# Kernel tuning notes

Hardware: AMD Instinct MI355X
Metric: run time of the kernel (lower is better)

The kernel has to match this reference:

```python
import jax, jax.numpy as jnp
import numpy as np

B, HGRID, D_MODEL = 4, 64, 96
D_INNER, D_STATE, DT_RANK, K = 192, 16, 6, 4
L = HGRID * HGRID


def setup_inputs() -> dict:
    key = jax.random.key(0)
    ks = jax.random.split(key, 12)
    C, N, R, D = D_INNER, D_STATE, DT_RANK, D_MODEL
    s = 0.02
    x = jax.random.normal(ks[0], (B, L, D), jnp.float32)
    in_proj_w = jax.random.normal(ks[1], (2 * C, D)) * s
    fft_w1 = jax.random.normal(ks[2], (C, C)) * s
    fft_b1 = jnp.zeros((C,))
    fft_w2 = jax.random.normal(ks[3], (C, C)) * s
    fft_b2 = jnp.zeros((C,))
    wave_w = jax.random.normal(ks[4], (C, C, 3, 3)) * s
    wave_b = jnp.zeros((C,))
    dw_w = jax.random.normal(ks[5], (C, 1, 3, 3)) * 0.1
    dw_b = jnp.zeros((C,))
    sym_w = jnp.asarray(0.3, jnp.float32)
    x_proj_w = jax.random.normal(ks[6], (K, R + 2 * N, C)) * s
    dt_std = R ** -0.5
    dt_w = jax.random.uniform(ks[7], (K, C, R), minval=-dt_std, maxval=dt_std)
    dt = jnp.exp(jax.random.uniform(ks[8], (K, C)) * (np.log(0.1) - np.log(0.001)) + np.log(0.001))
    dt = jnp.maximum(dt, 1e-4)
    dt_b = dt + jnp.log(-jnp.expm1(-dt))  # inverse softplus init as in dt_init
    A_logs = jnp.log(jnp.tile(jnp.arange(1, N + 1, dtype=jnp.float32), (K * C, 1)))  # [K*C, N]
    Ds = jnp.ones((K * C,))
    out_norm_g = jnp.ones((C,))
    out_norm_b = jnp.zeros((C,))
    out_proj_w = jax.random.normal(ks[9], (D, C)) * s
    rms_w = jnp.ones((D,))
    return dict(x=x, in_proj_w=in_proj_w, fft_w1=fft_w1, fft_b1=fft_b1, fft_w2=fft_w2,
                fft_b2=fft_b2, wave_w=wave_w, wave_b=wave_b, dw_w=dw_w, dw_b=dw_b,
                sym_w=sym_w, x_proj_w=x_proj_w, dt_w=dt_w, dt_b=dt_b, A_logs=A_logs,
                Ds=Ds, out_norm_g=out_norm_g, out_norm_b=out_norm_b,
                out_proj_w=out_proj_w, rms_w=rms_w)


def _conv2d(x, w, b, groups=1):
    y = jax.lax.conv_general_dilated(x, w, (1, 1), 'SAME', feature_group_count=groups,
                                     dimension_numbers=('NCHW', 'OIHW', 'NCHW'))
    return y + b[None, :, None, None]


def _haar_dwt(x):
    # orthonormal single-level Haar on 2x2 blocks
    a = x[..., 0::2, 0::2]; b = x[..., 0::2, 1::2]
    c = x[..., 1::2, 0::2]; d = x[..., 1::2, 1::2]
    return ((a + b + c + d) * 0.5, (a - b + c - d) * 0.5,
            (a + b - c - d) * 0.5, (a - b - c + d) * 0.5)


def _haar_idwt(ll, lh, hl, hh):
    a = (ll + lh + hl + hh) * 0.5; b = (ll - lh + hl - hh) * 0.5
    c = (ll + lh - hl - hh) * 0.5; d = (ll - lh - hl + hh) * 0.5
    Bb, Cc, H2, W2 = ll.shape
    top = jnp.stack([a, b], -1).reshape(Bb, Cc, H2, 2 * W2)
    bot = jnp.stack([c, d], -1).reshape(Bb, Cc, H2, 2 * W2)
    return jnp.stack([top, bot], -2).reshape(Bb, Cc, 2 * H2, 2 * W2)


def _freq_model(x, fft_w1, fft_b1, fft_w2, fft_b2, wave_w, wave_b):
    Bb, C, H, W = x.shape
    xf = jnp.fft.rfft2(x, norm='ortho')
    m = jax.nn.gelu(jnp.einsum('bchw,oc->bohw', jnp.abs(xf), fft_w1)
                    + fft_b1[None, :, None, None], approximate=False)
    mag = jnp.einsum('bchw,oc->bohw', m, fft_w2) + fft_b2[None, :, None, None]
    x_fourier = jnp.fft.irfft2(mag * jnp.exp(1j * jnp.angle(xf)), s=(H, W), norm='ortho')
    ll, lh, hl, hh = _haar_dwt(x)
    lh = _conv2d(lh, wave_w, wave_b)
    hl = _conv2d(hl, wave_w, wave_b)
    hh = _conv2d(hh, wave_w, wave_b)
    x_wavelet = _haar_idwt(ll, lh, hl, hh)
    return x + x_fourier + x_wavelet


def _selective_scan(xs, delta, A, Bs, Cs, Ds):
    # xs/delta: [B,K,C,L]; A: [K,C,N]; Bs/Cs: [B,K,N,L]; Ds: [K,C]
    Bb, Kk, C, Ll = xs.shape
    N = A.shape[-1]
    u_t = jnp.moveaxis(xs, -1, 0)     # [L,B,K,C]
    d_t = jnp.moveaxis(delta, -1, 0)
    B_t = jnp.moveaxis(Bs, -1, 0)     # [L,B,K,N]
    C_t = jnp.moveaxis(Cs, -1, 0)

    def step(h, inp):
        u, dd, bb, cc = inp
        h = jnp.exp(dd[..., None] * A) * h + (dd * u)[..., None] * bb[:, :, None, :]
        return h, jnp.einsum('bkcn,bkn->bkc', h, cc)

    h0 = jnp.zeros((Bb, Kk, C, N), xs.dtype)
    _, ys = jax.lax.scan(step, h0, (u_t, d_t, B_t, C_t))
    return jnp.moveaxis(ys, 0, -1) + xs * Ds[None, :, :, None]


def _forward(x, in_proj_w, fft_w1, fft_b1, fft_w2, fft_b2, wave_w, wave_b, dw_w, dw_b,
             sym_w, x_proj_w, dt_w, dt_b, A_logs, Ds, out_norm_g, out_norm_b,
             out_proj_w, rms_w):
    Bb, Ll, D = x.shape
    H = W = HGRID
    C, N, R = D_INNER, D_STATE, DT_RANK
    # RMSNorm (residual pre-norm)
    xn = x * jax.lax.rsqrt(jnp.mean(x * x, -1, keepdims=True) + 1e-5) * rms_w
    xz = xn.reshape(Bb, H, W, D) @ in_proj_w.T            # [B,H,W,2C]
    xi, z = jnp.split(xz, 2, axis=-1)
    xc = jnp.transpose(xi, (0, 3, 1, 2))                  # NCHW
    xc = xc + _freq_model(xc, fft_w1, fft_b1, fft_w2, fft_b2, wave_w, wave_b)
    a = jax.nn.silu(_conv2d(xc, dw_w, dw_b, groups=C))    # depthwise 3x3
    # 4-direction sequences
    x_flat = a.reshape(Bb, C, Ll)
    x_t = jnp.transpose(a, (0, 1, 3, 2)).reshape(Bb, C, Ll)
    xs = jnp.stack([x_flat, x_t, x_flat[..., ::-1], x_t[..., ::-1]], axis=1)  # [B,4,C,L]
    x_dbl = jnp.einsum('bkdl,kcd->bkcl', xs, x_proj_w)
    dts, Bs, Cs = jnp.split(x_dbl, [R, R + N], axis=2)
    dts = jnp.einsum('bkrl,kdr->bkdl', dts, dt_w)
    delta = jax.nn.softplus(dts + dt_b[None, :, :, None])
    A = -jnp.exp(A_logs).reshape(K, C, N)
    out_y = _selective_scan(xs, delta, A, Bs, Cs, Ds.reshape(K, C))  # [B,4,C,L]
    wh = jnp.transpose(out_y[:, 1].reshape(Bb, C, W, H), (0, 1, 3, 2)).reshape(Bb, C, Ll)
    iwh = jnp.transpose(out_y[:, 3, :, ::-1].reshape(Bb, C, W, H), (0, 1, 3, 2)).reshape(Bb, C, Ll)
    y = out_y[:, 0] + out_y[:, 2, :, ::-1] + wh + iwh     # [B,C,L]
    # lightweight symmetry enhancement
    y4 = y.reshape(Bb, C, H, W)
    wgt = jax.nn.sigmoid(sym_w)
    enh = y4 * (1 - wgt) + 0.5 * (y4 + y4[..., ::-1]) * wgt
    yf = y + 0.2 * enh.reshape(Bb, C, Ll)
    yf = jnp.transpose(yf, (0, 2, 1)).reshape(Bb, H, W, C)
    # LayerNorm
    mu = yf.mean(-1, keepdims=True)
    var = ((yf - mu) ** 2).mean(-1, keepdims=True)
    yn = (yf - mu) * jax.lax.rsqrt(var + 1e-5) * out_norm_g + out_norm_b
    out = (yn * jax.nn.silu(z)) @ out_proj_w.T
    return out.reshape(Bb, Ll, D) + x  # residual


def reference(x, in_proj_w, fft_w1, fft_b1, fft_w2, fft_b2, wave_w, wave_b, dw_w, dw_b,
              sym_w, x_proj_w, dt_w, dt_b, A_logs, Ds, out_norm_g, out_norm_b,
              out_proj_w, rms_w):
    return _forward(x, in_proj_w, fft_w1, fft_b1, fft_w2, fft_b2, wave_w, wave_b,
                    dw_w, dw_b, sym_w, x_proj_w, dt_w, dt_b, A_logs, Ds,
                    out_norm_g, out_norm_b, out_proj_w, rms_w)
```

## Files before the change

### kernel.cpp

```cpp
#include <hip/hip_runtime.h>
#include <hip/hip_bf16.h>

#define CI 192
#define LL_ 4096

typedef __bf16 v8bf __attribute__((ext_vector_type(8)));
typedef float  v4f  __attribute__((ext_vector_type(4)));
typedef float  v8f  __attribute__((ext_vector_type(8)));
typedef unsigned short v8us __attribute__((ext_vector_type(8)));

__device__ __forceinline__ unsigned short f2bf(float v){
  unsigned int u = __float_as_uint(v);
  return (unsigned short)((u + 0x7FFFu + ((u >> 16) & 1u)) >> 16);
}

__global__ __launch_bounds__(256) void k_zero(float* __restrict__ p, int n){
  int i = blockIdx.x*256 + threadIdx.x;
  if (i < n) p[i] = 0.f;
}

__global__ __launch_bounds__(256) void k_rms_inproj(const float* __restrict__ x,
    const float* __restrict__ rmsw, const float* __restrict__ ipw,
    float* __restrict__ xc, float* __restrict__ zT){
  int og = blockIdx.x & 7; int lt = (blockIdx.x >> 3) & 63; int b = blockIdx.x >> 9;
  int l0 = lt << 6;
  __shared__ float xt[64][97];
  __shared__ float wt[96*48];
  __shared__ float rr[64];
  __shared__ float rw[96];
  int tid = threadIdx.x;
  for (int idx = tid; idx < 6144; idx += 256){ int r = idx/96, d = idx - r*96;
    xt[r][d] = x[((size_t)b*4096 + l0 + r)*96 + d]; }
  if (tid < 96) rw[tid] = rmsw[tid];
  int o0 = og*48;
  for (int idx = tid; idx < 4608; idx += 256){ int o = idx%48, d = idx/48;
    wt[d*48 + o] = ipw[(size_t)(o0 + o)*96 + d]; }
  __syncthreads();
  if (tid < 64){
    float s = 0.f;
    for (int d = 0; d < 96; d++){ float v = xt[tid][d]; s += v*v; }
    rr[tid] = rsqrtf(s*(1.0f/96.0f) + 1e-5f);
  }
  __syncthreads();
  for (int idx = tid; idx < 6144; idx += 256){ int r = idx/96, d = idx - r*96;
    xt[r][d] *= rr[r]*rw[d]; }
  __syncthreads();
  int l = tid & 63, grp = tid >> 6;
  float acc[12];
  #pragma unroll
  for (int j = 0; j < 12; j++) acc[j] = 0.f;
  for (int d = 0; d < 96; d++){
    float xv = xt[l][d];
    const float* wr = &wt[d*48 + grp*12];
    #pragma unroll
    for (int j = 0; j < 12; j += 4){
      float4 w4 = *(const float4*)&wr[j];
      acc[j]   += xv*w4.x; acc[j+1] += xv*w4.y;
      acc[j+2] += xv*w4.z; acc[j+3] += xv*w4.w;
    }
  }
  #pragma unroll
  for (int j = 0; j < 12; j++){
    int o = o0 + grp*12 + j;
    if (o < 192) xc[((size_t)b*192 + o)*4096 + l0 + l] = acc[j];
    else         zT[((size_t)b*192 + (o-192))*4096 + l0 + l] = acc[j];
  }
}

__global__ __launch_bounds__(256) void k_dft_fwd(const float* __restrict__ xc,
    float* __restrict__ fre, float* __restrict__ fim, float* __restrict__ fab,
    float* __restrict__ ll, float* __restrict__ lh, float* __restrict__ hl, float* __restrict__ hh){
  int plane = blockIdx.x;
  __shared__ float sxT[64*65];
  __shared__ float t1r[64*34], t1i[64*34];
  __shared__ float tabr[16], tabi[16];
  __shared__ float ct64[64], st64[64];
  int tid = threadIdx.x;
  const float* X = xc + (size_t)plane*4096;
  for (int i = tid; i < 4096; i += 256){ int h = i >> 6, w = i & 63; sxT[w*65 + h] = X[i]; }
  if (tid < 16){ tabr[tid] = cospif((float)tid/8.0f); tabi[tid] = -sinpif((float)tid/8.0f); }
  if (tid < 64){ ct64[tid] = cospif((float)tid/32.0f); st64[tid] = sinpif((float)tid/32.0f); }
  __syncthreads();
  {
    size_t qbase = (size_t)plane*1024;
    for (int idx = tid; idx < 1024; idx += 256){
      int y2 = idx >> 5, x2 = idx & 31;
      float a_ = sxT[(2*x2)*65 + 2*y2],     b_ = sxT[(2*x2+1)*65 + 2*y2];
      float c_ = sxT[(2*x2)*65 + 2*y2+1],   d_ = sxT[(2*x2+1)*65 + 2*y2+1];
      ll[qbase + idx] = (a_+b_+c_+d_)*0.5f; lh[qbase + idx] = (a_-b_+c_-d_)*0.5f;
      hl[qbase + idx] = (a_+b_-c_-d_)*0.5f; hh[qbase + idx] = (a_-b_-c_+d_)*0.5f;
    }
  }
  {
    int hp = tid & 31, g = tid >> 5;
    float a0r[4], a0i[4], a1r[4], a1i[4];
    #pragma unroll
    for (int j = 0; j < 4; j++){ a0r[j]=0.f; a0i[j]=0.f; a1r[j]=0.f; a1i[j]=0.f; }
    float s32_0 = 0.f, s32_1 = 0.f;
    for (int w = 0; w < 64; w++){
      float xv0 = sxT[w*65 + hp];
      float xv1 = sxT[w*65 + hp + 32];
      int m0 = (w*g) & 15;
      float twr = tabr[m0], twi = tabi[m0];
      int ms = w & 15;
      float str = tabr[ms], sti = tabi[ms];
      #pragma unroll
      for (int j = 0; j < 4; j++){
        a0r[j] += xv0*twr; a0i[j] += xv0*twi;
        a1r[j] += xv1*twr; a1i[j] += xv1*twi;
        float nr = twr*str - twi*sti;
        float ni = twr*sti + twi*str;
        twr = nr; twi = ni;
      }
      if (g == 0){ float sg = (w & 1) ? -1.f : 1.f; s32_0 += xv0*sg; s32_1 += xv1*sg; }
    }
    #pragma unroll
    for (int j = 0; j < 4; j++){
      int k = 4*g + j;
      t1r[hp*34 + k] = a0r[j];        t1i[hp*34 + k] = a0i[j];
      t1r[(hp+32)*34 + k] = a1r[j];   t1i[(hp+32)*34 + k] = a1i[j];
    }
    if (g == 0){
      t1r[hp*34 + 32] = s32_0;      t1i[hp*34 + 32] = 0.f;
      t1r[(hp+32)*34 + 32] = s32_1; t1i[(hp+32)*34 + 32] = 0.f;
    }
  }
  __syncthreads();
  {
    int fp = tid & 31, g = tid >> 5;
    float stepr = cospif((float)fp/32.0f), stepi = -sinpif((float)fp/32.0f);
    float a0r[4], a0i[4], a1r[4], a1i[4];
    #pragma unroll
    for (int j = 0; j < 4; j++){ a0r[j]=0.f; a0i[j]=0.f; a1r[j]=0.f; a1i[j]=0.f; }
    float b0r=0.f, b0i=0.f, b1r=0.f, b1i=0.f;
    for (int hb = 0; hb < 4; hb++){
      int m = ((hb*16)*fp) & 63;
      float twr = ct64[m], twi = -st64[m];
      for (int hh2 = 0; hh2 < 16; hh2++){
        int h = hb*16 + hh2;
        float sg = (h & 1) ? -1.f : 1.f;
        #pragma unroll
        for (int j = 0; j < 4; j++){
          float Tr = t1r[h*34 + 4*g + j], Ti = t1i[h*34 + 4*g + j];
          float pr = Tr*twr - Ti*twi;
          float pi = Tr*twi + Ti*twr;
          a0r[j] += pr; a0i[j] += pi;
          a1r[j] += sg*pr; a1i[j] += sg*pi;
        }
        if (g == 0){
          float Tr = t1r[h*34 + 32], Ti = t1i[h*34 + 32];
          float pr = Tr*twr - Ti*twi, pi = Tr*twi + Ti*twr;
          b0r += pr; b0i += pi; b1r += sg*pr; b1i += sg*pi;
        }
        float nr = twr*stepr - twi*stepi, ni = twr*stepi + twi*stepr;
        twr = nr; twi = ni;
      }
    }
    size_t base = (size_t)plane*2112;
    #pragma unroll
    for (int j = 0; j < 4; j++){
      int k = 4*g + j;
      float r0 = a0r[j]*(1.f/64.f), i0 = a0i[j]*(1.f/64.f);
      float r1 = a1r[j]*(1.f/64.f), i1 = a1i[j]*(1.f/64.f);
      fre[base + fp*33 + k] = r0; fim[base + fp*33 + k] = i0;
      fab[base + fp*33 + k] = sqrtf(r0*r0 + i0*i0);
      fre[base + (fp+32)*33 + k] = r1; fim[base + (fp+32)*33 + k] = i1;
      fab[base + (fp+32)*33 + k] = sqrtf(r1*r1 + i1*i1);
    }
    if (g == 0){
      float r0 = b0r*(1.f/64.f), i0 = b0i*(1.f/64.f);
      float r1 = b1r*(1.f/64.f), i1 = b1i*(1.f/64.f);
      fre[base + fp*33 + 32] = r0; fim[base + fp*33 + 32] = i0;
      fab[base + fp*33 + 32] = sqrtf(r0*r0 + i0*i0);
      fre[base + (fp+32)*33 + 32] = r1; fim[base + (fp+32)*33 + 32] = i1;
      fab[base + (fp+32)*33 + 32] = sqrtf(r1*r1 + i1*i1);
    }
  }
}

__global__ __launch_bounds__(256) void k_cmix1(const float* __restrict__ fab,
    const float* __restrict__ w1, const float* __restrict__ b1, float* __restrict__ m){
  int bid = blockIdx.x;
  int pt = bid % 9; int og = (bid/9) % 24; int b = bid/216;
  int tid = threadIdx.x;
  int p = pt*256 + tid; bool act = p < 2112;
  __shared__ float wl[192*8];
  for (int idx = tid; idx < 1536; idx += 256){ int o = idx & 7, c = idx >> 3;
    wl[c*8 + o] = w1[(size_t)(og*8 + o)*192 + c]; }
  __syncthreads();
  float acc[8];
  #pragma unroll
  for (int o = 0; o < 8; o++) acc[o] = b1[og*8 + o];
  const float* xb = fab + (size_t)b*CI*2112 + p;
  for (int c = 0; c < 192; c++){
    float xv = act ? xb[(size_t)c*2112] : 0.f;
    float4 wa = *(const float4*)&wl[c*8];
    float4 wb4 = *(const float4*)&wl[c*8 + 4];
    acc[0] += xv*wa.x;  acc[1] += xv*wa.y;  acc[2] += xv*wa.z;  acc[3] += xv*wa.w;
    acc[4] += xv*wb4.x; acc[5] += xv*wb4.y; acc[6] += xv*wb4.z; acc[7] += xv*wb4.w;
  }
  if (act){
    #pragma unroll
    for (int o = 0; o < 8; o++){
      float a = acc[o];
      m[((size_t)b*192 + og*8 + o)*2112 + p] = 0.5f*a*(1.0f + erff(a*0.70710678118654752f));
    }
  }
}

__global__ __launch_bounds__(256) void k_cmix2(const float* __restrict__ m,
    const float* __restrict__ w2, const float* __restrict__ bi2,
    float* __restrict__ fre, float* __restrict__ fim, const float* __restrict__ fab){
  int bid = blockIdx.x;
  int pt = bid % 9; int og = (bid/9) % 24; int b = bid/216;
  int tid = threadIdx.x;
  int p = pt*256 + tid; bool act = p < 2112;
  __shared__ float wl[192*8];
  for (int idx = tid; idx < 1536; idx += 256){ int o = idx & 7, c = idx >> 3;
    wl[c*8 + o] = w2[(size_t)(og*8 + o)*192 + c]; }
  __syncthreads();
  float acc[8];
  #pragma unroll
  for (int o = 0; o < 8; o++) acc[o] = bi2[og*8 + o];
  const float* xb = m + (size_t)b*CI*2112 + p;
  for (int c = 0; c < 192; c++){
    float xv = act ? xb[(size_t)c*2112] : 0.f;
    float4 wa = *(const float4*)&wl[c*8];
    float4 wb4 = *(const float4*)&wl[c*8 + 4];
    acc[0] += xv*wa.x;  acc[1] += xv*wa.y;  acc[2] += xv*wa.z;  acc[3] += xv*wa.w;
    acc[4] += xv*wb4.x; acc[5] += xv*wb4.y; acc[6] += xv*wb4.z; acc[7] += xv*wb4.w;
  }
  if (act){
    #pragma unroll
    for (int o = 0; o < 8; o++){
      size_t id = ((size_t)b*192 + og*8 + o)*2112 + p;
      float ab = fab[id];
      float re, im;
      if (ab > 1e-30f){ float sc = acc[o]/ab; re = sc*fre[id]; im = sc*fim[id]; }
      else { re = acc[o]; im = 0.f; }
      fre[id] = re; fim[id] = im;
    }
  }
}

__global__ __launch_bounds__(256) void k_cvt_w(const float* __restrict__ ww,
    unsigned short* __restrict__ wqb2){
  int idx = blockIdx.x*256 + threadIdx.x;
  if (idx >= 331776) return;
  int ic = idx % 192; int rest = idx / 192;
  int oc = rest % 192; int q = rest / 192;
  wqb2[idx] = f2bf(ww[((size_t)oc*192 + ic)*9 + q]);
}

__global__ __launch_bounds__(256) void k_prep_lhT(const float* __restrict__ lhb,
    unsigned short* __restrict__ lhT){
  int id = blockIdx.x*256 + threadIdx.x;
  int pix = id & 1023;
  int icg = (id >> 10) % 24;
  int img = id / 24576;
  const float* s = lhb + (size_t)img*196608 + (size_t)(icg*8)*1024 + pix;
  v8us v;
  #pragma unroll
  for (int j = 0; j < 8; j++) v[j] = f2bf(s[(size_t)j*1024]);
  *(v8us*)&lhT[((size_t)img*1024 + pix)*192 + icg*8] = v;
}

__global__ __launch_bounds__(256) void k_wconv_mfma(const unsigned short* __restrict__ lhT,
    const unsigned short* __restrict__ wqb2, float* __restrict__ wnew){
  int bid = blockIdx.x;
  int nt = bid % 3; int mt = (bid/3) & 15; int img = bid/48;
  int o0 = nt*64;
  __shared__ __align__(16) unsigned short sm_us[26112];
  unsigned short* Aband = sm_us;
  float* T = (float*)sm_us;
  int tid = threadIdx.x;
  int lane = tid & 63, wv = tid >> 6;
  int quad = lane >> 4, n16 = lane & 15;
  const unsigned short* wrow = wqb2 + ((size_t)(o0 + 16*wv + n16))*192 + quad*8;
  v8us bcur[6], bnxt[6];
  #pragma unroll
  for (int icc = 0; icc < 6; icc++) bcur[icc] = *(const v8us*)&wrow[icc*32];
  for (int i = tid; i < 3264; i += 256) ((v8us*)sm_us)[i] = (v8us){0,0,0,0,0,0,0,0};
  __syncthreads();
  const unsigned short* base = lhT + (size_t)img*196608;
  for (int idx = tid; idx < 3072; idx += 256){
    int r = idx / 768; int t = idx - r*768;
    int pc = t / 24;   int icg = t - pc*24;
    int gr = 2*mt - 1 + r;
    if (gr >= 0 && gr < 32){
      v8us v = *(const v8us*)&base[((size_t)gr*32 + pc)*192 + icg*8];
      int pix = r*34 + 1 + pc;
      *(v8us*)&Aband[pix*192 + ((icg*8) ^ ((pix & 7) << 3))] = v;
    }
  }
  __syncthreads();
  v4f acc[4];
  #pragma unroll
  for (int t2 = 0; t2 < 4; t2++) acc[t2] = (v4f){0.f,0.f,0.f,0.f};
  #pragma unroll
  for (int q = 0; q < 9; q++){
    int ky = q/3, kx = q - ky*3;
    if (q < 8){
      #pragma unroll
      for (int icc = 0; icc < 6; icc++)
        bnxt[icc] = *(const v8us*)&wrow[(size_t)(q+1)*36864 + icc*32];
    }
    #pragma unroll
    for (int icc = 0; icc < 6; icc++){
      int c0 = icc*32;
      v8bf bv = __builtin_bit_cast(v8bf, bcur[icc]);
      #pragma unroll
      for (int t2 = 0; t2 < 4; t2++){
        int mm = t2*16 + n16;
        int pix = ((mm >> 5) + ky)*34 + (mm & 31) + kx;
        const unsigned short* Ap = &Aband[pix*192 + ((c0 + quad*8) ^ ((pix & 7) << 3))];
        v8bf av = __builtin_bit_cast(v8bf, *(const v8us*)Ap);
        acc[t2] = __builtin_amdgcn_mfma_f32_16x16x32_bf16(av, bv, acc[t2], 0, 0, 0);
      }
    }
    #pragma unroll
    for (int icc = 0; icc < 6; icc++) bcur[icc] = bnxt[icc];
  }
  __syncthreads();
  #pragma unroll
  for (int t2 = 0; t2 < 4; t2++)
    #pragma unroll
    for (int r = 0; r < 4; r++)
      T[(16*t2 + quad*4 + r)*65 + 16*wv + n16] = acc[t2][r];
  __syncthreads();
  float* outb = wnew + (size_t)img*196608;
  for (int idx = tid; idx < 4096; idx += 256){
    int mm = idx & 63, oc = idx >> 6;
    outb[(size_t)(o0 + oc)*1024 + mt*64 + mm] = T[mm*65 + oc];
  }
}

__global__ __launch_bounds__(256) void k_ifwd(const float* __restrict__ fre2,
    const float* __restrict__ fim2, const float* __restrict__ xc,
    const float* __restrict__ ll, const float* __restrict__ wnew, const float* __restrict__ wb,
    const float* __restrict__ dww, const float* __restrict__ dwb,
    float* __restrict__ ab, float* __restrict__ aT){
  int plane = blockIdx.x;
  int c = plane % 192;
  __shared__ float sm[12992];
  float* gr  = sm;
  float* gi  = sm + 2176;
  float* ur  = sm + 4352;
  float* ui  = sm + 6528;
  float* sx2 = sm + 8704;
  float* t64r = sm + 12864; float* t64i = sm + 12928;
  float* scratch = sm;
  int tid = threadIdx.x;
  for (int i = tid; i < 2112; i += 256){
    size_t o = (size_t)plane*2112 + i;
    int f = i/33, k = i - f*33;
    gr[f*34 + k] = fre2[o]; gi[f*34 + k] = fim2[o];
  }
  if (tid < 64){ t64r[tid] = cospif((float)tid/32.0f); t64i[tid] = sinpif((float)tid/32.0f); }
  __syncthreads();
  {
    int hp = tid & 31, g = tid >> 5;
    float stepr = cospif((float)hp/32.0f), stepi = sinpif((float)hp/32.0f);
    float a0r[4], a0i[4], a1r[4], a1i[4];
    #pragma unroll
    for (int j = 0; j < 4; j++){ a0r[j]=0.f; a0i[j]=0.f; a1r[j]=0.f; a1i[j]=0.f; }
    float b0r=0.f, b0i=0.f, b1r=0.f, b1i=0.f;
    for (int fb = 0; fb < 4; fb++){
      int m = ((fb*16)*hp) & 63;
      float twr = t64r[m], twi = t64i[m];
      for (int ff = 0; ff < 16; ff++){
        int f = fb*16 + ff;
        float sg = (f & 1) ? -1.f : 1.f;
        #pragma unroll
        for (int j = 0; j < 4; j++){
          float Gr = gr[f*34 + 4*g + j], Gi = gi[f*34 + 4*g + j];
          float pr = Gr*twr - Gi*twi;
          float pi = Gr*twi + Gi*twr;
          a0r[j] += pr; a0i[j] += pi;
          a1r[j] += sg*pr; a1i[j] += sg*pi;
        }
        if (g == 0){
          float Gr = gr[f*34 + 32], Gi = gi[f*34 + 32];
          float pr = Gr*twr - Gi*twi, pi = Gr*twi + Gi*twr;
          b0r += pr; b0i += pi; b1r += sg*pr; b1i += sg*pi;
        }
        float nr = twr*stepr - twi*stepi, ni = twr*stepi + twi*stepr;
        twr = nr; twi = ni;
      }
    }
    __syncthreads();
    #pragma unroll
    for (int j = 0; j < 4; j++){
      int k = 4*g + j;
      float ck = (k == 0) ? (1.f/64.f) : (2.f/64.f);
      ur[hp*34 + k] = a0r[j]*ck;       ui[hp*34 + k] = a0i[j]*ck;
      ur[(hp+32)*34 + k] = a1r[j]*ck;  ui[(hp+32)*34 + k] = a1i[j]*ck;
    }
    if (g == 0){
      ur[hp*34 + 32] = b0r*(1.f/64.f);      ui[hp*34 + 32] = b0i*(1.f/64.f);
      ur[(hp+32)*34 + 32] = b1r*(1.f/64.f); ui[(hp+32)*34 + 32] = b1i*(1.f/64.f);
    }
  }
  __syncthreads();
  {
    int h = tid & 63, wg = tid >> 6;
    v8f accL = (v8f)0.f, accH = (v8f)0.f, twr, twi, sr, si;
    #pragma unroll
    for (int j = 0; j < 8; j++){
      int wl = 8*wg + j;
      sr[j] = t64r[wl]; si[j] = t64i[wl];
      twr[j] = 1.f; twi[j] = 0.f;
    }
    float acc32 = 0.f;
    for (int k = 0; k <= 32; k++){
      float Ur = ur[h*34 + k], Ui = ui[h*34 + k];
      if (wg == 0) acc32 += (k & 1) ? -Ur : Ur;
      v8f p = Ur*twr, q = Ui*twi;
      accL += p - q;
      accH += p + q;
      v8f nr = twr*sr - twi*si;
      v8f ni = twr*si + twi*sr;
      twr = nr; twi = ni;
    }
    #pragma unroll
    for (int j = 0; j < 8; j++){
      int wl = 8*wg + j;
      sx2[h*65 + wl] = accL[j];
      if (wl == 0) sx2[h*65 + 32] = acc32;
      else         sx2[h*65 + 64 - wl] = accH[j];
    }
  }
  __syncthreads();
  float bia = wb[c];
  for (int p = tid; p < 4096; p += 256){
    int h = p >> 6, w = p & 63;
    size_t q = (size_t)plane*1024 + (size_t)(h >> 1)*32 + (w >> 1);
    float LLv = ll[q];
    float LH = wnew[q] + bia;
    float HL = wnew[786432 + q] + bia;
    float HH = wnew[1572864 + q] + bia;
    float v;
    bool hb = (h & 1), wbit = (w & 1);
    if (!hb && !wbit)      v = (LLv + LH + HL + HH)*0.5f;
    else if (!hb && wbit)  v = (LLv - LH + HL - HH)*0.5f;
    else if (hb && !wbit)  v = (LLv + LH - HL - HH)*0.5f;
    else                   v = (LLv - LH - HL + HH)*0.5f;
    sx2[h*65 + w] = 2.0f*xc[(size_t)plane*4096 + p] + sx2[h*65 + w] + v;
  }
  __syncthreads();
  float wk[9];
  #pragma unroll
  for (int q = 0; q < 9; q++) wk[q] = dww[c*9 + q];
  float dbv = dwb[c];
  for (int p = tid; p < 4096; p += 256){
    int h = p >> 6, w = p & 63;
    float acc = dbv;
    #pragma unroll
    for (int ky = 0; ky < 3; ky++){
      int yy = h + ky - 1; if (yy < 0 || yy > 63) continue;
      #pragma unroll
      for (int kx = 0; kx < 3; kx++){
        int xx = w + kx - 1; if (xx < 0 || xx > 63) continue;
        acc += sx2[yy*65 + xx]*wk[ky*3 + kx];
      }
    }
    scratch[h*65 + w] = acc / (1.f + __expf(-acc));
  }
  __syncthreads();
  float* abp = ab + (size_t)plane*4096;
  float* aTp = aT + (size_t)plane*4096;
  for (int p = tid; p < 4096; p += 256){
    abp[p] = scratch[(p >> 6)*65 + (p & 63)];
    aTp[p] = scratch[(p & 63)*65 + (p >> 6)];
  }
}

__global__ __launch_bounds__(256) void k_xproj(const float* __restrict__ ab,
    const float* __restrict__ aT, const float* __restrict__ xpw,
    float* __restrict__ Bsb, float* __restrict__ Csb, float* __restrict__ dlsb,
    float* __restrict__ xsb){
  int bid = blockIdx.x;
  int s = bid & 63; int k = (bid >> 6) & 3; int b = bid >> 8;
  int tid = threadIdx.x;
  __shared__ float als[192][65];
  __shared__ float dls[6][64];
  int l0 = s << 6;
  const float* src = (k & 1) ? aT : ab;
  bool rev = (k >= 2);
  for (int idx = tid; idx < 3072; idx += 256){
    int d = idx >> 4, i4 = idx & 15;
    const float* rowp = src + ((size_t)b*192 + d)*4096;
    if (!rev){
      float4 v = *(const float4*)&rowp[l0 + 4*i4];
      als[d][4*i4+0] = v.x; als[d][4*i4+1] = v.y;
      als[d][4*i4+2] = v.z; als[d][4*i4+3] = v.w;
    } else {
      float4 v = *(const float4*)&rowp[4092 - l0 - 4*i4];
      als[d][4*i4+0] = v.w; als[d][4*i4+1] = v.z;
      als[d][4*i4+2] = v.y; als[d][4*i4+3] = v.x;
    }
  }
  __syncthreads();
  {
    int i = tid & 63, wg = tid >> 6;
    const float* wr[10];
    #pragma unroll
    for (int r = 0; r < 10; r++){
      int cp = wg + 4*r; if (cp > 37) cp = 37;
      int off = __builtin_amdgcn_readfirstlane((k*38 + cp)*192);
      wr[r] = xpw + off;
    }
    float acc[10];
    #pragma unroll
    for (int r = 0; r < 10; r++) acc[r] = 0.f;
    for (int d = 0; d < 192; d++){
      float v = als[d][i];
      #pragma unroll
      for (int r = 0; r < 10; r++) acc[r] += v*wr[r][d];
    }
    #pragma unroll
    for (int r = 0; r < 10; r++){
      int cp = wg + 4*r;
      if (cp > 37) continue;
      if (cp < 6) dls[cp][i] = acc[r];
      else if (cp < 22) Bsb[((size_t)(b*4 + k)*16 + (cp - 6 ))*4096 + l0 + i] = acc[r];
      else              Csb[((size_t)(b*4 + k)*16 + (cp - 22))*4096 + l0 + i] = acc[r];
    }
  }
  size_t xbase = ((size_t)(b*4 + k)*4096 + l0)*192;
  for (int j = tid; j < 3072; j += 256){
    int i = j / 48, c4 = (j - (j/48)*48)*4;
    float4 v;
    v.x = als[c4+0][i]; v.y = als[c4+1][i];
    v.z = als[c4+2][i]; v.w = als[c4+3][i];
    *(float4*)&xsb[xbase + (size_t)i*192 + c4] = v;
  }
  __syncthreads();
  size_t dbase = (size_t)((b*4 + k)*64 + s)*384;
  for (int j = tid; j < 384; j += 256){
    int i = j/6, r = j - i*6;
    dlsb[dbase + j] = dls[r][i];
  }
}

__global__ __launch_bounds__(192) void k_scanA(const float* __restrict__ xsb,
    const float* __restrict__ dlsb, const float* __restrict__ Bsb,
    const float* __restrict__ dtw, const float* __restrict__ dtb,
    const float* __restrict__ alog, float* __restrict__ Pb, float* __restrict__ Qb){
  int bid = blockIdx.x; int s = bid & 63; int k = (bid >> 6) & 3; int b = bid >> 8;
  int c = threadIdx.x; int bk = b*4 + k;
  __shared__ float sdl[384];
  __shared__ float sB[16][64];
  size_t dbase = (size_t)(bk*64 + s)*384;
  for (int j = c; j < 384; j += 192) sdl[j] = dlsb[dbase + j];
  for (int j = c; j < 1024; j += 192){ int n = j >> 6, i = j & 63;
    sB[n][i] = Bsb[((size_t)bk*16 + n)*4096 + (s << 6) + i]; }
  __syncthreads();
  float A[16], P[16], Q[16];
  const float* arow = alog + ((size_t)k*192 + c)*16;
  bool fast = true;
  #pragma unroll
  for (int n = 0; n < 16; n++){
    A[n] = -__expf(arow[n]); P[n] = 1.f; Q[n] = 0.f;
    if (fabsf(A[n] + (float)(n+1)) > 1e-3f) fast = false;
  }
  float dw[6];
  #pragma unroll
  for (int r = 0; r < 6; r++) dw[r] = dtw[((size_t)k*192 + c)*6 + r];
  float db = dtb[k*192 + c];
  const float* xrow = xsb + ((size_t)bk*4096 + (s << 6))*192 + c;
  if (fast){
    for (int i = 0; i < 64; i++){
      float u = xrow[(size_t)i*192];
      float acc = db;
      #pragma unroll
      for (int r = 0; r < 6; r++) acc += sdl[i*6 + r]*dw[r];
      float ec = __expf(fminf(acc, 80.f));
      float dl = __logf(1.f + ec);
      float e1 = __builtin_amdgcn_rcpf(1.f + ec);
      float du = dl*u;
      float e = 1.f;
      #pragma unroll
      for (int n = 0; n < 16; n++){
        e *= e1;
        P[n] *= e;
        Q[n] = Q[n]*e + du*sB[n][i];
      }
    }
  } else {
    for (int i = 0; i < 64; i++){
      float u = xrow[(size_t)i*192];
      float acc = db;
      #pragma unroll
      for (int r = 0; r < 6; r++) acc += sdl[i*6 + r]*dw[r];
      float ec = __expf(fminf(acc, 80.f));
      float dl = __logf(1.f + ec);
      float du = dl*u;
      #pragma unroll
      for (int n = 0; n < 16; n++){
        float e = __expf(dl*A[n]);
        P[n] *= e;
        Q[n] = Q[n]*e + du*sB[n][i];
      }
    }
  }
  size_t pbase = ((size_t)(bk*64 + s)*16)*192 + c;
  #pragma unroll
  for (int n = 0; n < 16; n++){ Pb[pbase + (size_t)n*192] = P[n]; Qb[pbase + (size_t)n*192] = Q[n]; }
}

__global__ __launch_bounds__(256) void k_scanB(float* __restrict__ Pb,
    const float* __restrict__ Qb){
  int id = blockIdx.x*256 + threadIdx.x;
  int c = id % 192; int rest = id / 192; int n = rest % 16; int bk = rest / 16;
  float h = 0.f;
  for (int s = 0; s < 64; s++){
    size_t o = (((size_t)bk*64 + s)*16 + n)*192 + c;
    float P = Pb[o], Q = Qb[o];
    Pb[o] = h;
    h = P*h + Q;
  }
}

__global__ __launch_bounds__(192) void k_scanC_buf(const float* __restrict__ xsb,
    const float* __restrict__ dlsb, const float* __restrict__ Bsb, const float* __restrict__ Csb,
    const float* __restrict__ hinb, const float* __restrict__ dtw, const float* __restrict__ dtb,
    const float* __restrict__ alog, const float* __restrict__ Dsp, float* __restrict__ Y){
  int bid = blockIdx.x; int s = bid & 63; int k = (bid >> 6) & 3; int b = bid >> 8;
  int c = threadIdx.x; int bk = b*4 + k;
  __shared__ float sdl[384];
  __shared__ float sB[16][64];
  __shared__ float sC[16][64];
  size_t dbase = (size_t)(bk*64 + s)*384;
  for (int j = c; j < 384; j += 192) sdl[j] = dlsb[dbase + j];
  for (int j = c; j < 1024; j += 192){ int n = j >> 6, i = j & 63;
    size_t o = ((size_t)bk*16 + n)*4096 + (s << 6) + i;
    sB[n][i] = Bsb[o]; sC[n][i] = Csb[o]; }
  __syncthreads();
  float A[16], h[16];
  const float* arow = alog + ((size_t)k*192 + c)*16;
  bool fast = true;
  #pragma unroll
  for (int n = 0; n < 16; n++){
    A[n] = -__expf(arow[n]);
    if (fabsf(A[n] + (float)(n+1)) > 1e-3f) fast = false;
  }
  size_t hbase = ((size_t)(bk*64 + s)*16)*192 + c;
  #pragma unroll
  for (int n = 0; n < 16; n++) h[n] = hinb[hbase + (size_t)n*192];
  float dw[6];
  #pragma unroll
  for (int r = 0; r < 6; r++) dw[r] = dtw[((size_t)k*192 + c)*6 + r];
  float db = dtb[k*192 + c];
  float Dc = Dsp[k*192 + c];
  const float* xrow = xsb + ((size_t)bk*4096 + (s << 6))*192 + c;
  float* Yk = Y + (((size_t)bk*4096 + (s << 6))*192) + c;
  if (fast){
    for (int i = 0; i < 64; i++){
      float u = xrow[(size_t)i*192];
      float acc = db;
      #pragma unroll
      for (int r = 0; r < 6; r++) acc += sdl[i*6 + r]*dw[r];
      float ec = __expf(fminf(acc, 80.f));
      float dl = __logf(1.f + ec);
      float e1 = __builtin_amdgcn_rcpf(1.f + ec);
      float du = dl*u;
      float e = 1.f;
      float y = 0.f;
      #pragma unroll
      for (int n = 0; n < 16; n++){
        e *= e1;
        h[n] = h[n]*e + du*sB[n][i];
        y += h[n]*sC[n][i];
      }
      Yk[(size_t)i*192] = y + u*Dc;
    }
  } else {
    for (int i = 0; i < 64; i++){
      float u = xrow[(size_t)i*192];
      float acc = db;
      #pragma unroll
      for (int r = 0; r < 6; r++) acc += sdl[i*6 + r]*dw[r];
      float ec = __expf(fminf(acc, 80.f));
      float dl = __logf(1.f + ec);
      float du = dl*u;
      float y = 0.f;
      #pragma unroll
      for (int n = 0; n < 16; n++){
        float e = __expf(dl*A[n]);
        h[n] = h[n]*e + du*sB[n][i];
        y += h[n]*sC[n][i];
      }
      Yk[(size_t)i*192] = y + u*Dc;
    }
  }
}

__global__ __launch_bounds__(192) void k_scanC_atom(const float* __restrict__ xsb,
    const float* __restrict__ dlsb, const float* __restrict__ Bsb, const float* __restrict__ Csb,
    const float* __restrict__ hinb, const float* __restrict__ dtw, const float* __restrict__ dtb,
    const float* __restrict__ alog, const float* __restrict__ Dsp, float* __restrict__ yb){
  int bid = blockIdx.x; int s = bid & 63; int k = (bid >> 6) & 3; int b = bid >> 8;
  int c = threadIdx.x; int bk = b*4 + k;
  __shared__ float sdl[384];
  __shared__ float sB[16][64];
  __shared__ float sC[16][64];
  size_t dbase = (size_t)(bk*64 + s)*384;
  for (int j = c; j < 384; j += 192) sdl[j] = dlsb[dbase + j];
  for (int j = c; j < 1024; j += 192){ int n = j >> 6, i = j & 63;
    size_t o = ((size_t)bk*16 + n)*4096 + (s << 6) + i;
    sB[n][i] = Bsb[o]; sC[n][i] = Csb[o]; }
  __syncthreads();
  float A[16], h[16];
  const float* arow = alog + ((size_t)k*192 + c)*16;
  bool fast = true;
  #pragma unroll
  for (int n = 0; n < 16; n++){
    A[n] = -__expf(arow[n]);
    if (fabsf(A[n] + (float)(n+1)) > 1e-3f) fast = false;
  }
  size_t hbase = ((size_t)(bk*64 + s)*16)*192 + c;
  #pragma unroll
  for (int n = 0; n < 16; n++) h[n] = hinb[hbase + (size_t)n*192];
  float dw[6];
  #pragma unroll
  for (int r = 0; r < 6; r++) dw[r] = dtw[((size_t)k*192 + c)*6 + r];
  float db = dtb[k*192 + c];
  float Dc = Dsp[k*192 + c];
  const float* xrow = xsb + ((size_t)bk*4096 + (s << 6))*192 + c;
  int p0, pst;
  if (k == 0){ p0 = s << 6;        pst = 1;  }
  else if (k == 1){ p0 = s;        pst = 64; }
  else if (k == 2){ p0 = 4095 - (s << 6); pst = -1; }
  else { p0 = 4095 - s;            pst = -64; }
  for (int i = 0; i < 64; i++){
    float u = xrow[(size_t)i*192];
    float acc = db;
    #pragma unroll
    for (int r = 0; r < 6; r++) acc += sdl[i*6 + r]*dw[r];
    float ec = __expf(fminf(acc, 80.f));
    float dl = __logf(1.f + ec);
    float du = dl*u;
    float y = 0.f;
    if (fast){
      float e1 = __builtin_amdgcn_rcpf(1.f + ec);
      float e = 1.f;
      #pragma unroll
      for (int n = 0; n < 16; n++){
        e *= e1;
        h[n] = h[n]*e + du*sB[n][i];
        y += h[n]*sC[n][i];
      }
    } else {
      #pragma unroll
      for (int n = 0; n < 16; n++){
        float e = __expf(dl*A[n]);
        h[n] = h[n]*e + du*sB[n][i];
        y += h[n]*sC[n][i];
      }
    }
    y += u*Dc;
    atomicAdd(&yb[((size_t)b*4096 + p0 + pst*i)*192 + c], y);
  }
}

__global__ __launch_bounds__(256) void k_enh(const float* __restrict__ yb,
    const float* __restrict__ symw, float* __restrict__ yfb){
  int id = blockIdx.x*256 + threadIdx.x;
  int c = id % 192; int rest = id / 192; int l = rest & 4095; int b = rest >> 12;
  int w = l & 63; int lr = (l | 63) - w;
  float v  = yb[id];
  float vr = yb[(((size_t)b << 12) + lr)*192 + c];
  float wg = 1.f/(1.f + __expf(-symw[0]));
  float enh = v*(1.f - wg) + 0.5f*(v + vr)*wg;
  yfb[id] = v + 0.2f*enh;
}

__global__ __launch_bounds__(256) void k_final_comb(const float* __restrict__ Y,
    const float* __restrict__ symw, const float* __restrict__ zT,
    const float* __restrict__ g, const float* __restrict__ bta,
    const float* __restrict__ opw, const float* __restrict__ x, float* __restrict__ out){
  int og = blockIdx.x & 1; int lt = (blockIdx.x >> 1) & 127; int b = blockIdx.x >> 8;
  int l0 = lt << 5;
  __shared__ float sv[32][193];
  __shared__ float wt[192*48];
  __shared__ float sg[192], sb2[192];
  __shared__ float smu[32], srs[32];
  int tid = threadIdx.x;
  const size_t S = (size_t)4096*192;
  float wg = 1.f/(1.f + __expf(-symw[0]));
  for (int idx = tid; idx < 6144; idx += 256){
    int r = idx/192, cc = idx - r*192;
    int l = l0 + r;
    int w = l & 63, hh2 = l >> 6;
    int lr  = (l & ~63) | (63 - w);
    int p1  = (w << 6) | hh2;
    int p1r = ((63 - w) << 6) | hh2;
    size_t base = (size_t)(b*4)*S + cc;
    float v  = Y[base + (size_t)l*192]
             + Y[base + S + (size_t)p1*192]
             + Y[base + 2*S + (size_t)(4095 - l)*192]
             + Y[base + 3*S + (size_t)(4095 - p1)*192];
    float vr = Y[base + (size_t)lr*192]
             + Y[base + S + (size_t)p1r*192]
             + Y[base + 2*S + (size_t)(4095 - lr)*192]
             + Y[base + 3*S + (size_t)(4095 - p1r)*192];
    float enh = v*(1.f - wg) + 0.5f*(v + vr)*wg;
    sv[r][cc] = v + 0.2f*enh;
  }
  if (tid < 192){ sg[tid] = g[tid]; sb2[tid] = bta[tid]; }
  int o0 = og*48;
  for (int idx = tid; idx < 9216; idx += 256){ int o = idx % 48, c = idx/48;
    wt[c*48 + o] = opw[(size_t)(o0 + o)*192 + c]; }
  __syncthreads();
  if (tid < 32){
    float s1 = 0.f, s2 = 0.f;
    for (int c = 0; c < 192; c++){ float v = sv[tid][c]; s1 += v; s2 += v*v; }
    float mu = s1*(1.0f/192.0f);
    smu[tid] = mu; srs[tid] = rsqrtf(s2*(1.0f/192.0f) - mu*mu + 1e-5f);
  }
  __syncthreads();
  for (int idx = tid; idx < 6144; idx += 256){ int l = idx & 31, c = idx >> 5;
    float zv = zT[((size_t)b*192 + c)*4096 + l0 + l];
    float v = sv[l][c];
    float yn = (v - smu[l])*srs[l]*sg[c] + sb2[c];
    sv[l][c] = yn * (zv/(1.f + __expf(-zv)));
  }
  __syncthreads();
  int l = tid & 31, grp = tid >> 5;
  float acc[6];
  #pragma unroll
  for (int j = 0; j < 6; j++) acc[j] = 0.f;
  for (int c = 0; c < 192; c++){
    float svv = sv[l][c];
    const float* wr = &wt[c*48 + grp*6];
    #pragma unroll
    for (int j = 0; j < 6; j += 2){
      float2 w2 = *(const float2*)&wr[j];
      acc[j]   += svv*w2.x; acc[j+1] += svv*w2.y;
    }
  }
  size_t ob = ((size_t)b*4096 + l0 + l)*96 + o0 + grp*6;
  #pragma unroll
  for (int j = 0; j < 6; j++) acc[j] += x[ob + j];
  #pragma unroll
  for (int j = 0; j < 6; j += 2){
    float2 v2; v2.x = acc[j]; v2.y = acc[j+1];
    *(float2*)&out[ob + j] = v2;
  }
}

__global__ __launch_bounds__(256) void k_final(const float* __restrict__ yf,
    const float* __restrict__ zT, const float* __restrict__ g, const float* __restrict__ bta,
    const float* __restrict__ opw, const float* __restrict__ x, float* __restrict__ out){
  int og = blockIdx.x & 1; int lt = (blockIdx.x >> 1) & 127; int b = blockIdx.x >> 8;
  int l0 = lt << 5;
  __shared__ float sv[32][193];
  __shared__ float wt[192*48];
  __shared__ float sg[192], sb2[192];
  __shared__ float smu[32], srs[32];
  int tid = threadIdx.x;
  for (int idx = tid; idx < 6144; idx += 256){ int r = idx/192, c = idx - r*192;
    sv[r][c] = yf[((size_t)b*4096 + l0 + r)*192 + c]; }
  if (tid < 192){ sg[tid] = g[tid]; sb2[tid] = bta[tid]; }
  int o0 = og*48;
  for (int idx = tid; idx < 9216; idx += 256){ int o = idx % 48, c = idx/48;
    wt[c*48 + o] = opw[(size_t)(o0 + o)*192 + c]; }
  __syncthreads();
  if (tid < 32){
    float s1 = 0.f, s2 = 0.f;
    for (int c = 0; c < 192; c++){ float v = sv[tid][c]; s1 += v; s2 += v*v; }
    float mu = s1*(1.0f/192.0f);
    smu[tid] = mu; srs[tid] = rsqrtf(s2*(1.0f/192.0f) - mu*mu + 1e-5f);
  }
  __syncthreads();
  for (int idx = tid; idx < 6144; idx += 256){ int l = idx & 31, c = idx >> 5;
    float zv = zT[((size_t)b*192 + c)*4096 + l0 + l];
    float v = sv[l][c];
    float yn = (v - smu[l])*srs[l]*sg[c] + sb2[c];
    sv[l][c] = yn * (zv/(1.f + __expf(-zv)));
  }
  __syncthreads();
  int l = tid & 31, grp = tid >> 5;
  float acc[6];
  #pragma unroll
  for (int j = 0; j < 6; j++) acc[j] = 0.f;
  for (int c = 0; c < 192; c++){
    float svv = sv[l][c];
    const float* wr = &wt[c*48 + grp*6];
    #pragma unroll
    for (int j = 0; j < 6; j += 2){
      float2 w2 = *(const float2*)&wr[j];
      acc[j]   += svv*w2.x; acc[j+1] += svv*w2.y;
    }
  }
  size_t ob = ((size_t)b*4096 + l0 + l)*96 + o0 + grp*6;
  #pragma unroll
  for (int j = 0; j < 6; j++) acc[j] += x[ob + j];
  #pragma unroll
  for (int j = 0; j < 6; j += 2){
    float2 v2; v2.x = acc[j]; v2.y = acc[j+1];
    *(float2*)&out[ob + j] = v2;
  }
}

extern "C" void kernel_launch(void* const* d_in, const int* in_sizes, int n_in,
                              void* d_out, int out_size, void* d_ws, size_t ws_size,
                              hipStream_t stream){
  (void)in_sizes; (void)n_in; (void)out_size;
  const float* ix   = (const float*)d_in[0];
  const float* ipw  = (const float*)d_in[1];
  const float* fw1  = (const float*)d_in[2];
  const float* fb1  = (const float*)d_in[3];
  const float* fw2  = (const float*)d_in[4];
  const float* fb2  = (const float*)d_in[5];
  const float* ww   = (const float*)d_in[6];
  const float* wb   = (const float*)d_in[7];
  const float* dww  = (const float*)d_in[8];
  const float* dwb  = (const float*)d_in[9];
  const float* symw = (const float*)d_in[10];
  const float* xpw  = (const float*)d_in[11];
  const float* dtw  = (const float*)d_in[12];
  const float* dtb  = (const float*)d_in[13];
  const float* alog = (const float*)d_in[14];
  const float* Dsp  = (const float*)d_in[15];
  const float* ong  = (const float*)d_in[16];
  const float* onb  = (const float*)d_in[17];
  const float* opw  = (const float*)d_in[18];
  const float* rmsw = (const float*)d_in[19];

  float* W = (float*)d_ws;
  const size_t SZ_BLC = 3145728, SZ_F = 1622016, SZ_H = 786432;
  float* zT  = W;
  float* ab  = zT + SZ_BLC;
  float* R0  = ab + SZ_BLC;
  float* xc    = R0;
  float* fre   = xc  + SZ_BLC;
  float* fim   = fre + SZ_F;
  float* fab   = fim + SZ_F;
  float* mb    = fab + SZ_F;
  float* llb   = mb  + SZ_F;
  float* lhb   = llb + SZ_H;
  float* wnew  = lhb + 3*SZ_H;
  unsigned short* wqb2 = (unsigned short*)(wnew + 2359296);
  unsigned short* lhT  = wqb2 + 331776;
  float* Bsb  = R0;
  float* Csb  = Bsb + 1048576;
  float* dlsb = Csb + 1048576;
  float* xsb  = dlsb + 393216;
  float* Pb   = xsb + 12582912;
  float* aT   = Pb;
  float* Qb   = Pb + SZ_BLC;
  float* Yb   = Qb;
  float* ybA  = Qb + SZ_BLC;
  float* yfb  = xsb;

  const size_t NEED_BIG = (size_t)(6291456 + 30801920) * 4;
  bool bigws = (ws_size >= NEED_BIG);

  hipLaunchKernelGGL(k_rms_inproj, dim3(2048),   dim3(256), 0, stream, ix, rmsw, ipw, xc, zT);
  hipLaunchKernelGGL(k_dft_fwd,    dim3(4*192),  dim3(256), 0, stream, xc, fre, fim, fab,
                     llb, lhb, lhb + SZ_H, lhb + 2*SZ_H);
  hipLaunchKernelGGL(k_cvt_w,      dim3(1296),   dim3(256), 0, stream, ww, wqb2);
  hipLaunchKernelGGL(k_prep_lhT,   dim3(1152),   dim3(256), 0, stream, lhb, lhT);
  hipLaunchKernelGGL(k_cmix1,      dim3(864),    dim3(256), 0, stream, fab, fw1, fb1, mb);
  hipLaunchKernelGGL(k_cmix2,      dim3(864),    dim3(256), 0, stream, mb, fw2, fb2, fre, fim, fab);
  hipLaunchKernelGGL(k_wconv_mfma, dim3(576),    dim3(256), 0, stream, lhT, wqb2, wnew);
  hipLaunchKernelGGL(k_ifwd,       dim3(768),    dim3(256), 0, stream, fre, fim, xc, llb, wnew, wb, dww, dwb, ab, aT);
  hipLaunchKernelGGL(k_xproj,      dim3(1024),   dim3(256), 0, stream, ab, aT, xpw, Bsb, Csb, dlsb, xsb);
  hipLaunchKernelGGL(k_scanA,      dim3(1024),   dim3(192), 0, stream, xsb, dlsb, Bsb, dtw, dtb, alog, Pb, Qb);
  hipLaunchKernelGGL(k_scanB,      dim3(192),    dim3(256), 0, stream, Pb, Qb);
  if (bigws){
    hipLaunchKernelGGL(k_scanC_buf,  dim3(1024), dim3(192), 0, stream, xsb, dlsb, Bsb, Csb, Pb, dtw, dtb, alog, Dsp, Yb);
    hipLaunchKernelGGL(k_final_comb, dim3(1024), dim3(256), 0, stream, Yb, symw, zT, ong, onb, opw, ix, (float*)d_out);
  } else {
    hipLaunchKernelGGL(k_zero,       dim3(12288), dim3(256), 0, stream, ybA, (int)SZ_BLC);
    hipLaunchKernelGGL(k_scanC_atom, dim3(1024),  dim3(192), 0, stream, xsb, dlsb, Bsb, Csb, Pb, dtw, dtb, alog, Dsp, ybA);
    hipLaunchKernelGGL(k_enh,        dim3(12288), dim3(256), 0, stream, ybA, symw, yfb);
    hipLaunchKernelGGL(k_final,      dim3(1024),  dim3(256), 0, stream, yfb, zT, ong, onb, opw, ix, (float*)d_out);
  }
}
```

Measured before the change: 584.5 us.

## Pair mirrored columns in final combine and halve xproj shared tile

k_final_comb now groups each block's 32 positions as 16 columns plus their horizontal mirrors. The symmetry term can then come from rows already in shared memory instead of eight extra gathers per element, and the four-direction sum is loaded with float4. k_xproj splits its 192-channel shared tile into two 96-channel halves, which lowers shared memory use and could allow more blocks per CU, at the cost of an extra sync round. The final kernel's zT reads and output writes become non-contiguous through an index map.

```diff
diff --git a/kernel.cpp b/kernel.cpp
--- a/kernel.cpp
+++ b/kernel.cpp
@@ -482,64 +482,67 @@
   int bid = blockIdx.x;
   int s = bid & 63; int k = (bid >> 6) & 3; int b = bid >> 8;
   int tid = threadIdx.x;
-  __shared__ float als[192][65];
+  __shared__ float als[96][65];
   __shared__ float dls[6][64];
   int l0 = s << 6;
   const float* src = (k & 1) ? aT : ab;
   bool rev = (k >= 2);
-  for (int idx = tid; idx < 3072; idx += 256){
-    int d = idx >> 4, i4 = idx & 15;
-    const float* rowp = src + ((size_t)b*192 + d)*4096;
-    if (!rev){
-      float4 v = *(const float4*)&rowp[l0 + 4*i4];
-      als[d][4*i4+0] = v.x; als[d][4*i4+1] = v.y;
-      als[d][4*i4+2] = v.z; als[d][4*i4+3] = v.w;
-    } else {
-      float4 v = *(const float4*)&rowp[4092 - l0 - 4*i4];
-      als[d][4*i4+0] = v.w; als[d][4*i4+1] = v.z;
-      als[d][4*i4+2] = v.y; als[d][4*i4+3] = v.x;
-    }
-  }
-  __syncthreads();
-  {
-    int i = tid & 63, wg = tid >> 6;
-    const float* wr[10];
-    #pragma unroll
-    for (int r = 0; r < 10; r++){
-      int cp = wg + 4*r; if (cp > 37) cp = 37;
-      int off = __builtin_amdgcn_readfirstlane((k*38 + cp)*192);
-      wr[r] = xpw + off;
-    }
-    float acc[10];
-    #pragma unroll
-    for (int r = 0; r < 10; r++) acc[r] = 0.f;
-    for (int d = 0; d < 192; d++){
+  int i = tid & 63, wg = tid >> 6;
+  const float* wr[10];
+  #pragma unroll
+  for (int r = 0; r < 10; r++){
+    int cp = wg + 4*r; if (cp > 37) cp = 37;
+    int off = __builtin_amdgcn_readfirstlane((k*38 + cp)*192);
+    wr[r] = xpw + off;
+  }
+  float acc[10];
+  #pragma unroll
+  for (int r = 0; r < 10; r++) acc[r] = 0.f;
+  size_t xbase = ((size_t)(b*4 + k)*4096 + l0)*192;
+  #pragma unroll
+  for (int half = 0; half < 2; half++){
+    int d0 = half*96;
+    for (int idx = tid; idx < 1536; idx += 256){
+      int d = idx >> 4, i4 = idx & 15;
+      const float* rowp = src + ((size_t)b*192 + d0 + d)*4096;
+      if (!rev){
+        float4 v = *(const float4*)&rowp[l0 + 4*i4];
+        als[d][4*i4+0] = v.x; als[d][4*i4+1] = v.y;
+        als[d][4*i4+2] = v.z; als[d][4*i4+3] = v.w;
+      } else {
+        float4 v = *(const float4*)&rowp[4092 - l0 - 4*i4];
+        als[d][4*i4+0] = v.w; als[d][4*i4+1] = v.z;
+        als[d][4*i4+2] = v.y; als[d][4*i4+3] = v.x;
+      }
+    }
+    __syncthreads();
+    for (int d = 0; d < 96; d++){
       float v = als[d][i];
       #pragma unroll
-      for (int r = 0; r < 10; r++) acc[r] += v*wr[r][d];
-    }
-    #pragma unroll
-    for (int r = 0; r < 10; r++){
-      int cp = wg + 4*r;
-      if (cp > 37) continue;
-      if (cp < 6) dls[cp][i] = acc[r];
-      else if (cp < 22) Bsb[((size_t)(b*4 + k)*16 + (cp - 6 ))*4096 + l0 + i] = acc[r];
-      else              Csb[((size_t)(b*4 + k)*16 + (cp - 22))*4096 + l0 + i] = acc[r];
-    }
-  }
-  size_t xbase = ((size_t)(b*4 + k)*4096 + l0)*192;
-  for (int j = tid; j < 3072; j += 256){
-    int i = j / 48, c4 = (j - (j/48)*48)*4;
-    float4 v;
-    v.x = als[c4+0][i]; v.y = als[c4+1][i];
-    v.z = als[c4+2][i]; v.w = als[c4+3][i];
-    *(float4*)&xsb[xbase + (size_t)i*192 + c4] = v;
+      for (int r = 0; r < 10; r++) acc[r] += v*wr[r][d0 + d];
+    }
+    for (int idx = tid; idx < 1536; idx += 256){
+      int ii = idx / 24, cc = (idx - (idx/24)*24)*4;
+      float4 v;
+      v.x = als[cc+0][ii]; v.y = als[cc+1][ii];
+      v.z = als[cc+2][ii]; v.w = als[cc+3][ii];
+      *(float4*)&xsb[xbase + (size_t)ii*192 + d0 + cc] = v;
+    }
+    __syncthreads();
+  }
+  #pragma unroll
+  for (int r = 0; r < 10; r++){
+    int cp = wg + 4*r;
+    if (cp > 37) continue;
+    if (cp < 6) dls[cp][i] = acc[r];
+    else if (cp < 22) Bsb[((size_t)(b*4 + k)*16 + (cp - 6 ))*4096 + l0 + i] = acc[r];
+    else              Csb[((size_t)(b*4 + k)*16 + (cp - 22))*4096 + l0 + i] = acc[r];
   }
   __syncthreads();
   size_t dbase = (size_t)((b*4 + k)*64 + s)*384;
   for (int j = tid; j < 384; j += 256){
-    int i = j/6, r = j - i*6;
-    dlsb[dbase + j] = dls[r][i];
+    int ii = j/6, r = j - ii*6;
+    dlsb[dbase + j] = dls[r][ii];
   }
 }
 
@@ -781,37 +784,57 @@
     const float* __restrict__ g, const float* __restrict__ bta,
     const float* __restrict__ opw, const float* __restrict__ x, float* __restrict__ out){
   int og = blockIdx.x & 1; int lt = (blockIdx.x >> 1) & 127; int b = blockIdx.x >> 8;
-  int l0 = lt << 5;
+  int h = lt >> 1, wsel = lt & 1;
   __shared__ float sv[32][193];
   __shared__ float wt[192*48];
   __shared__ float sg[192], sb2[192];
   __shared__ float smu[32], srs[32];
+  __shared__ int lmap[32];
   int tid = threadIdx.x;
   const size_t S = (size_t)4096*192;
   float wg = 1.f/(1.f + __expf(-symw[0]));
-  for (int idx = tid; idx < 6144; idx += 256){
-    int r = idx/192, cc = idx - r*192;
-    int l = l0 + r;
-    int w = l & 63, hh2 = l >> 6;
-    int lr  = (l & ~63) | (63 - w);
-    int p1  = (w << 6) | hh2;
-    int p1r = ((63 - w) << 6) | hh2;
-    size_t base = (size_t)(b*4)*S + cc;
-    float v  = Y[base + (size_t)l*192]
-             + Y[base + S + (size_t)p1*192]
-             + Y[base + 2*S + (size_t)(4095 - l)*192]
-             + Y[base + 3*S + (size_t)(4095 - p1)*192];
-    float vr = Y[base + (size_t)lr*192]
-             + Y[base + S + (size_t)p1r*192]
-             + Y[base + 2*S + (size_t)(4095 - lr)*192]
-             + Y[base + 3*S + (size_t)(4095 - p1r)*192];
-    float enh = v*(1.f - wg) + 0.5f*(v + vr)*wg;
-    sv[r][cc] = v + 0.2f*enh;
+  if (tid < 32){
+    int r = tid;
+    int w = (r < 16) ? (wsel*16 + r) : (63 - wsel*16 - (r - 16));
+    lmap[r] = h*64 + w;
+  }
+  for (int idx = tid; idx < 1536; idx += 256){
+    int r = idx / 48, c4 = (idx - (idx/48)*48)*4;
+    int w = (r < 16) ? (wsel*16 + r) : (63 - wsel*16 - (r - 16));
+    int l = h*64 + w;
+    int p1 = (w << 6) | h;
+    size_t base = (size_t)(b*4)*S + c4;
+    float4 v0 = *(const float4*)&Y[base + (size_t)l*192];
+    float4 v1 = *(const float4*)&Y[base + S + (size_t)p1*192];
+    float4 v2 = *(const float4*)&Y[base + 2*S + (size_t)(4095 - l)*192];
+    float4 v3 = *(const float4*)&Y[base + 3*S + (size_t)(4095 - p1)*192];
+    sv[r][c4+0] = v0.x + v1.x + v2.x + v3.x;
+    sv[r][c4+1] = v0.y + v1.y + v2.y + v3.y;
+    sv[r][c4+2] = v0.z + v1.z + v2.z + v3.z;
+    sv[r][c4+3] = v0.w + v1.w + v2.w + v3.w;
   }
   if (tid < 192){ sg[tid] = g[tid]; sb2[tid] = bta[tid]; }
   int o0 = og*48;
   for (int idx = tid; idx < 9216; idx += 256){ int o = idx % 48, c = idx/48;
     wt[c*48 + o] = opw[(size_t)(o0 + o)*192 + c]; }
+  __syncthreads();
+  float yreg[24];
+  #pragma unroll
+  for (int t = 0; t < 24; t++){
+    int idx = tid + t*256;
+    int r = idx / 192, cc = idx - r*192;
+    int rp = (r < 16) ? r + 16 : r - 16;
+    float v = sv[r][cc], vp = sv[rp][cc];
+    float enh = v*(1.f - wg) + 0.5f*(v + vp)*wg;
+    yreg[t] = v + 0.2f*enh;
+  }
+  __syncthreads();
+  #pragma unroll
+  for (int t = 0; t < 24; t++){
+    int idx = tid + t*256;
+    int r = idx / 192, cc = idx - r*192;
+    sv[r][cc] = yreg[t];
+  }
   __syncthreads();
   if (tid < 32){
     float s1 = 0.f, s2 = 0.f;
@@ -821,7 +844,7 @@
   }
   __syncthreads();
   for (int idx = tid; idx < 6144; idx += 256){ int l = idx & 31, c = idx >> 5;
-    float zv = zT[((size_t)b*192 + c)*4096 + l0 + l];
+    float zv = zT[((size_t)b*192 + c)*4096 + lmap[l]];
     float v = sv[l][c];
     float yn = (v - smu[l])*srs[l]*sg[c] + sb2[c];
     sv[l][c] = yn * (zv/(1.f + __expf(-zv)));
@@ -840,7 +863,7 @@
       acc[j]   += svv*w2.x; acc[j+1] += svv*w2.y;
     }
   }
-  size_t ob = ((size_t)b*4096 + l0 + l)*96 + o0 + grp*6;
+  size_t ob = ((size_t)b*4096 + lmap[l])*96 + o0 + grp*6;
   #pragma unroll
   for (int j = 0; j < 6; j++) acc[j] += x[ob + j];
   #pragma unroll
```

Result: faster. 557.1 us (-4.7%).
